# Kernel tuning notes

Measured on AMD Instinct MI355X. Metric: run time of the kernel, lower is better.

The kernel has to match this reference:

```python
import jax, jax.numpy as jnp
import numpy as np

DIVERSITY_RATE = 0.5


def setup_inputs() -> dict:
    key = jax.random.key(0)
    k1, k2 = jax.random.split(key)
    # model log-probabilities at current step: (bsz, beam, vocab)
    lprobs = jax.nn.log_softmax(
        jax.random.normal(k1, (128, 5, 50257), dtype=jnp.float32), axis=-1
    )
    # historical hypothesis scores: (bsz, beam, step)
    scores = jax.random.normal(k2, (128, 5, 10), dtype=jnp.float32)
    return {"lprobs": lprobs, "scores": scores, "step": 10}


def reference(lprobs, scores, step):
    bsz, beam_size, vocab_size = lprobs.shape
    k = min(beam_size * 2, beam_size * vocab_size - 1)  # = 10 here

    # step > 0 path: accumulate running score of each hypothesis
    lp = lprobs + scores[:, :, step - 1][:, :, None]  # (bsz, beam, vocab)

    # 1/ per-beam top-k over vocab (vectorized over all beams at once)
    s, idx = jax.lax.top_k(lp, k)  # (bsz, beam, k); idx already < vocab (fmod no-op)

    # 2/,3/ intra-sibling ordering -> rank penalty (rank r gets r*rate)
    sibling_score = jnp.arange(1, k + 1, dtype=lp.dtype) * DIVERSITY_RATE  # (k,)
    s = s - sibling_score  # broadcast over (bsz, beam, k)

    # 4/ final top-k over all beam*k candidates
    indices = idx.reshape(bsz, beam_size * k)
    final_scores, flat_pos = jax.lax.top_k(s.reshape(bsz, beam_size * k), k)
    final_beams = flat_pos // k  # which input beam each winner came from
    final_indices = jnp.take_along_axis(indices, flat_pos, axis=1)  # vocab ids

    return final_scores, final_indices, final_beams
```

## Files before the change

kernel.cpp:

```cpp
#include <hip/hip_runtime.h>
#include <hip/hip_bf16.h>
#include <math.h>
#include <stdint.h>


#define BS    256
#define KK    10
#define BEAM  5
#define CS    7168
#define NSLOT 7
#define CAP   2048
#define FCAP  2048

typedef unsigned long long u64;

__device__ __forceinline__ uint32_t ford(float x) {
    uint32_t u = __float_as_uint(x);
    return (u & 0x80000000u) ? ~u : (u | 0x80000000u);
}
__device__ __forceinline__ float funord(uint32_t u) {
    return __uint_as_float((u & 0x80000000u) ? (u & 0x7fffffffu) : ~u);
}

__device__ __forceinline__ void insert10(u64 (&key)[KK], u64 k) {
    if (k > key[KK - 1]) {
#pragma unroll
        for (int j = KK - 1; j >= 1; --j)
            key[j] = (k > key[j - 1]) ? key[j - 1] : ((k > key[j]) ? k : key[j]);
        if (k > key[0]) key[0] = k;
    }
}

__global__ __launch_bounds__(BS) void dss_chunk_topk(
    const float* __restrict__ lprobs,
    const float* __restrict__ scores,
    const int*   __restrict__ step_ptr,
    int vocab, int sdim, int nc,
    u64* __restrict__ ws_keys)
{
    const int chunk = blockIdx.x;
    const int row   = blockIdx.y;
    const int tid   = threadIdx.x;
    const int lane  = tid & 63;
    const int step  = step_ptr[0];
    const float bias = scores[(size_t)row * sdim + (step - 1)];

    const int c0 = chunk * CS;
    int len = vocab - c0; if (len > CS) len = CS;
    const float* cp = lprobs + (size_t)row * vocab + c0;

    __shared__ u64  cand[CAP];
    __shared__ int  s_cnt;
    __shared__ float s_tau;

    int pre = (4 - (int)(((uintptr_t)cp >> 2) & 3)) & 3;
    if (pre > len) pre = len;
    const float4* g4 = (const float4*)(cp + pre);
    const int nvec = (len - pre) >> 2;
    const int done = pre + 4 * nvec;
    const int rem  = len - done;

    float4 v[NSLOT];
    float m = -INFINITY;
#pragma unroll
    for (int i = 0; i < NSLOT; ++i) {
        int idx = tid + (i << 8);
        if (idx < nvec) {
            float4 x = g4[idx];
            x.x += bias; x.y += bias; x.z += bias; x.w += bias;
            v[i] = x;
            m = fmaxf(m, fmaxf(fmaxf(x.x, x.y), fmaxf(x.z, x.w)));
        } else {
            v[i].x = -INFINITY; v[i].y = -INFINITY; v[i].z = -INFINITY; v[i].w = -INFINITY;
        }
    }
    float xv = -INFINITY; int xi = -1;
    if (tid < pre)                        { xi = tid;            xv = cp[xi] + bias; }
    else if (tid >= 4 && tid < 4 + rem)   { xi = done + tid - 4; xv = cp[xi] + bias; }
    m = fmaxf(m, xv);

    if (tid == 0) s_cnt = 0;

    if (tid < 64) {
        float s = m;
#pragma unroll
        for (int k2 = 2; k2 <= 64; k2 <<= 1) {
#pragma unroll
            for (int j = k2 >> 1; j >= 1; j >>= 1) {
                float p = __shfl_xor(s, j);
                bool lower   = (lane & j) == 0;
                bool dirDesc = (lane & k2) == 0;
                s = (dirDesc == lower) ? fmaxf(s, p) : fminf(s, p);
            }
        }
        if (lane == 9) s_tau = s;
    }
    __syncthreads();
    const float tau = s_tau;

    auto app = [&](float x, int j) {
        if (j < len) {
            int p = atomicAdd(&s_cnt, 1);
            if (p < CAP) cand[p] = ((u64)ford(x) << 32) | (uint32_t)~(c0 + j);
        }
    };
#pragma unroll
    for (int i = 0; i < NSLOT; ++i) {
        int base = pre + ((tid + (i << 8)) << 2);
        if (v[i].x >= tau) app(v[i].x, base + 0);
        if (v[i].y >= tau) app(v[i].y, base + 1);
        if (v[i].z >= tau) app(v[i].z, base + 2);
        if (v[i].w >= tau) app(v[i].w, base + 3);
    }
    if (xi >= 0 && xv >= tau) app(xv, xi);
    __syncthreads();

    if (tid < 64) {
        int n = s_cnt; if (n > CAP) n = CAP;
        u64* outp = ws_keys + ((size_t)row * nc + chunk) * KK;
        if (n <= 64) {
            u64 k = (lane < n) ? cand[lane] : 0;
#pragma unroll
            for (int k2 = 2; k2 <= 64; k2 <<= 1) {
#pragma unroll
                for (int j = k2 >> 1; j >= 1; j >>= 1) {
                    u64 p = __shfl_xor(k, j);
                    bool lower   = (lane & j) == 0;
                    bool dirDesc = (lane & k2) == 0;
                    bool wantMax = (dirDesc == lower);
                    k = wantMax ? (k > p ? k : p) : (k < p ? k : p);
                }
            }
            if (lane < KK) outp[lane] = k;
        } else {
            u64 key[KK];
#pragma unroll
            for (int j = 0; j < KK; ++j) key[j] = 0;
            for (int i = lane; i < n; i += 64) insert10(key, cand[i]);
#pragma unroll
            for (int r = 0; r < KK; ++r) {
                u64 rv = key[0]; int rl = lane;
#pragma unroll
                for (int o = 32; o >= 1; o >>= 1) {
                    u64 ov = __shfl_xor(rv, o);
                    int ol = __shfl_xor(rl, o);
                    if (ov > rv || (ov == rv && ol < rl)) { rv = ov; rl = ol; }
                }
                if (lane == rl) {
#pragma unroll
                    for (int j = 0; j < KK - 1; ++j) key[j] = key[j + 1];
                    key[KK - 1] = 0;
                }
                if (lane == 0) outp[r] = rv;
            }
        }
    }
}

__global__ __launch_bounds__(BS) void dss_row_topk(
    const float* __restrict__ lprobs,
    const float* __restrict__ scores,
    const int*   __restrict__ step_ptr,
    int vocab, int sdim,
    u64* __restrict__ ws_keys)
{
    const int row = blockIdx.x;
    const int tid = threadIdx.x;
    const int step = step_ptr[0];
    const float bias = scores[(size_t)row * sdim + (step - 1)];
    const float* rp = lprobs + (size_t)row * vocab;

    __shared__ u64  cand[FCAP];
    __shared__ u64  skey[BS * KK];
    __shared__ int  cnt;
    __shared__ float sh_tau;

    int pre = (4 - (int)(((uintptr_t)rp >> 2) & 3)) & 3;
    if (pre > vocab) pre = vocab;
    const float4* p4 = (const float4*)(rp + pre);
    const int nvec = (vocab - pre) >> 2;
    const int done = pre + 4 * nvec;
    const int rem  = vocab - done;

    float m = -INFINITY;
    if (tid < pre) m = rp[tid] + bias;
    for (int t = tid; t < nvec; t += BS) {
        float4 x = p4[t];
        m = fmaxf(m, fmaxf(fmaxf(x.x + bias, x.y + bias), fmaxf(x.z + bias, x.w + bias)));
    }
    if (tid < rem) m = fmaxf(m, rp[done + tid] + bias);

    skey[tid * KK] = ((u64)ford(m) << 32) | (uint32_t)~tid;
#pragma unroll
    for (int j = 1; j < KK; ++j) skey[tid * KK + j] = 0;
    if (tid == 0) cnt = 0;
    __syncthreads();
    for (int off = BS / 2; off >= 1; off >>= 1) {
        if (tid < off) {
            const int pa = tid * KK, pb = (tid + off) * KK;
            u64 mk[KK]; int ia = 0, ib = 0;
#pragma unroll
            for (int j = 0; j < KK; ++j) {
                u64 ka = skey[pa + ia], kb = skey[pb + ib];
                bool tA = (ka >= kb); mk[j] = tA ? ka : kb;
                if (tA) ++ia; else ++ib;
            }
#pragma unroll
            for (int j = 0; j < KK; ++j) skey[pa + j] = mk[j];
        }
        __syncthreads();
    }
    if (tid == 0) sh_tau = funord((uint32_t)(skey[9] >> 32));
    __syncthreads();
    const float tau = sh_tau;

    auto app = [&](float x, int i) {
        if (x >= tau) {
            int p = atomicAdd(&cnt, 1);
            if (p < FCAP) cand[p] = ((u64)ford(x) << 32) | (uint32_t)~i;
        }
    };
    if (tid < pre) app(rp[tid] + bias, tid);
    for (int t = tid; t < nvec; t += BS) {
        float4 x = p4[t];
        int base = pre + 4 * t;
        app(x.x + bias, base + 0); app(x.y + bias, base + 1);
        app(x.z + bias, base + 2); app(x.w + bias, base + 3);
    }
    if (tid < rem) app(rp[done + tid] + bias, done + tid);
    __syncthreads();

    const int n = (cnt < FCAP) ? cnt : FCAP;
    {
        u64 key[KK];
#pragma unroll
        for (int j = 0; j < KK; ++j) key[j] = 0;
        for (int i = tid; i < n; i += BS) insert10(key, cand[i]);
#pragma unroll
        for (int j = 0; j < KK; ++j) skey[tid * KK + j] = key[j];
    }
    __syncthreads();
    for (int off = BS / 2; off >= 1; off >>= 1) {
        if (tid < off) {
            const int pa = tid * KK, pb = (tid + off) * KK;
            u64 mk[KK]; int ia = 0, ib = 0;
#pragma unroll
            for (int j = 0; j < KK; ++j) {
                u64 ka = skey[pa + ia], kb = skey[pb + ib];
                bool tA = (ka >= kb); mk[j] = tA ? ka : kb;
                if (tA) ++ia; else ++ib;
            }
#pragma unroll
            for (int j = 0; j < KK; ++j) skey[pa + j] = mk[j];
        }
        __syncthreads();
    }
    if (tid < KK) ws_keys[(size_t)row * KK + tid] = skey[tid];
}

__global__ __launch_bounds__(BEAM * 64) void dss_final(
    const u64* __restrict__ ws_keys,
    float* __restrict__ out, int bsz, int nc)
{
    const int b    = blockIdx.x;
    const int beam = threadIdx.x >> 6;
    const int lane = threadIdx.x & 63;

    __shared__ float s_pen[BEAM * KK];
    __shared__ int   s_idx[BEAM * KK];

    const int ncand = nc * KK;
    const u64* kp = ws_keys + (size_t)(b * BEAM + beam) * ncand;
    u64 c0 = (lane < ncand) ? kp[lane] : 0;
    u64 c1 = (lane + 64 < ncand) ? kp[lane + 64] : 0;

#pragma unroll
    for (int r = 0; r < KK; ++r) {
        u64 my = (c0 > c1) ? c0 : c1;
        u64 rv = my; int rl = lane;
#pragma unroll
        for (int o = 32; o >= 1; o >>= 1) {
            u64 ov = __shfl_xor(rv, o);
            int ol = __shfl_xor(rl, o);
            if (ov > rv || (ov == rv && ol < rl)) { rv = ov; rl = ol; }
        }
        if (lane == rl) { if (c0 == rv) c0 = 0; else c1 = 0; }
        if (lane == 0) {
            s_pen[beam * KK + r] = funord((uint32_t)(rv >> 32)) - 0.5f * (float)(r + 1);
            s_idx[beam * KK + r] = (int)~(uint32_t)rv;
        }
    }
    __syncthreads();

    if (threadIdx.x < 64) {
        float v = -INFINITY; int vidx = 0;
        if (lane < BEAM * KK) { v = s_pen[lane]; vidx = s_idx[lane]; }
        float* out_scores  = out;
        float* out_indices = out + (size_t)bsz * KK;
        float* out_beams   = out + 2 * (size_t)bsz * KK;
        for (int o = 0; o < KK; ++o) {
            float rv = v; int rp = lane;
#pragma unroll
            for (int off = 32; off >= 1; off >>= 1) {
                float ov = __shfl_xor(rv, off);
                int   op = __shfl_xor(rp, off);
                if (ov > rv || (ov == rv && op < rp)) { rv = ov; rp = op; }
            }
            int widx = __shfl(vidx, rp);
            if (lane == 0) {
                out_scores [b * KK + o] = rv;
                out_indices[b * KK + o] = (float)widx;
                out_beams  [b * KK + o] = (float)(rp / KK);
            }
            if (lane == rp) v = -INFINITY;
        }
    }
}

extern "C" void kernel_launch(void* const* d_in, const int* in_sizes, int n_in,
                              void* d_out, int out_size, void* d_ws, size_t ws_size,
                              hipStream_t stream)
{
    const float* lprobs = (const float*)d_in[0];
    const float* scores = (const float*)d_in[1];
    const int*   step   = (const int*)d_in[2];

    const int bsz   = 128;
    const int rows  = bsz * BEAM;
    const int vocab = in_sizes[0] / rows;
    const int sdim  = in_sizes[1] / rows;

    u64* ws_keys = (u64*)d_ws;

    int nc = (vocab + CS - 1) / CS;
    if (ws_size < (size_t)rows * nc * KK * sizeof(u64)) nc = 1;

    if (nc > 1) {
        dss_chunk_topk<<<dim3(nc, rows), BS, 0, stream>>>(
            lprobs, scores, step, vocab, sdim, nc, ws_keys);
    } else {
        dss_row_topk<<<rows, BS, 0, stream>>>(lprobs, scores, step, vocab, sdim, ws_keys);
    }
    dss_final<<<bsz, BEAM * 64, 0, stream>>>(ws_keys, (float*)d_out, bsz, nc);
}
```

Measured before the change: 211.9 us.

## Replace bitonic sorts and shuffle argmax loops with rank-counting selection

```diff
diff --git a/kernel.cpp b/kernel.cpp
--- a/kernel.cpp
+++ b/kernel.cpp
@@ -9,7 +9,7 @@
 #define BEAM  5
 #define CS    7168
 #define NSLOT 7
-#define CAP   2048
+#define CAP   1024
 #define FCAP  2048
 
 typedef unsigned long long u64;
@@ -51,7 +51,6 @@
 
     __shared__ u64  cand[CAP];
     __shared__ int  s_cnt;
-    __shared__ float s_tau;
 
     int pre = (4 - (int)(((uintptr_t)cp >> 2) & 3)) & 3;
     if (pre > len) pre = len;
@@ -81,22 +80,17 @@
 
     if (tid == 0) s_cnt = 0;
 
-    if (tid < 64) {
-        float s = m;
-#pragma unroll
-        for (int k2 = 2; k2 <= 64; k2 <<= 1) {
-#pragma unroll
-            for (int j = k2 >> 1; j >= 1; j >>= 1) {
-                float p = __shfl_xor(s, j);
-                bool lower   = (lane & j) == 0;
-                bool dirDesc = (lane & k2) == 0;
-                s = (dirDesc == lower) ? fmaxf(s, p) : fminf(s, p);
-            }
-        }
-        if (lane == 9) s_tau = s;
-    }
-    __syncthreads();
-    const float tau = s_tau;
+    int r = 0;
+    const int mb = __float_as_int(m);
+    for (int j = 0; j < 64; ++j) {
+        float vj = __int_as_float(__builtin_amdgcn_readlane(mb, j));
+        r += (vj > m || (vj == m && j < lane)) ? 1 : 0;
+    }
+    u64 msk = __ballot(r == 9);
+    int src = __ffsll((long long)msk) - 1;
+    const float tau = __int_as_float(__builtin_amdgcn_readlane(mb, src));
+
+    __syncthreads();
 
     auto app = [&](float x, int j) {
         if (j < len) {
@@ -115,45 +109,13 @@
     if (xi >= 0 && xv >= tau) app(xv, xi);
     __syncthreads();
 
-    if (tid < 64) {
-        int n = s_cnt; if (n > CAP) n = CAP;
-        u64* outp = ws_keys + ((size_t)row * nc + chunk) * KK;
-        if (n <= 64) {
-            u64 k = (lane < n) ? cand[lane] : 0;
-#pragma unroll
-            for (int k2 = 2; k2 <= 64; k2 <<= 1) {
-#pragma unroll
-                for (int j = k2 >> 1; j >= 1; j >>= 1) {
-                    u64 p = __shfl_xor(k, j);
-                    bool lower   = (lane & j) == 0;
-                    bool dirDesc = (lane & k2) == 0;
-                    bool wantMax = (dirDesc == lower);
-                    k = wantMax ? (k > p ? k : p) : (k < p ? k : p);
-                }
-            }
-            if (lane < KK) outp[lane] = k;
-        } else {
-            u64 key[KK];
-#pragma unroll
-            for (int j = 0; j < KK; ++j) key[j] = 0;
-            for (int i = lane; i < n; i += 64) insert10(key, cand[i]);
-#pragma unroll
-            for (int r = 0; r < KK; ++r) {
-                u64 rv = key[0]; int rl = lane;
-#pragma unroll
-                for (int o = 32; o >= 1; o >>= 1) {
-                    u64 ov = __shfl_xor(rv, o);
-                    int ol = __shfl_xor(rl, o);
-                    if (ov > rv || (ov == rv && ol < rl)) { rv = ov; rl = ol; }
-                }
-                if (lane == rl) {
-#pragma unroll
-                    for (int j = 0; j < KK - 1; ++j) key[j] = key[j + 1];
-                    key[KK - 1] = 0;
-                }
-                if (lane == 0) outp[r] = rv;
-            }
-        }
+    int n = s_cnt; if (n > CAP) n = CAP;
+    u64* outp = ws_keys + ((size_t)row * nc + chunk) * KK;
+    for (int t = tid; t < n; t += BS) {
+        u64 k = cand[t];
+        int rk = 0;
+        for (int j = 0; j < n; ++j) rk += (cand[j] > k) ? 1 : 0;
+        if (rk < KK) outp[rk] = k;
     }
 }
 
@@ -258,61 +220,46 @@
     if (tid < KK) ws_keys[(size_t)row * KK + tid] = skey[tid];
 }
 
-__global__ __launch_bounds__(BEAM * 64) void dss_final(
+__global__ __launch_bounds__(512) void dss_final(
     const u64* __restrict__ ws_keys,
     float* __restrict__ out, int bsz, int nc)
 {
-    const int b    = blockIdx.x;
-    const int beam = threadIdx.x >> 6;
-    const int lane = threadIdx.x & 63;
-
-    __shared__ float s_pen[BEAM * KK];
-    __shared__ int   s_idx[BEAM * KK];
-
-    const int ncand = nc * KK;
-    const u64* kp = ws_keys + (size_t)(b * BEAM + beam) * ncand;
-    u64 c0 = (lane < ncand) ? kp[lane] : 0;
-    u64 c1 = (lane + 64 < ncand) ? kp[lane + 64] : 0;
-
-#pragma unroll
-    for (int r = 0; r < KK; ++r) {
-        u64 my = (c0 > c1) ? c0 : c1;
-        u64 rv = my; int rl = lane;
-#pragma unroll
-        for (int o = 32; o >= 1; o >>= 1) {
-            u64 ov = __shfl_xor(rv, o);
-            int ol = __shfl_xor(rl, o);
-            if (ov > rv || (ov == rv && ol < rl)) { rv = ov; rl = ol; }
-        }
-        if (lane == rl) { if (c0 == rv) c0 = 0; else c1 = 0; }
-        if (lane == 0) {
-            s_pen[beam * KK + r] = funord((uint32_t)(rv >> 32)) - 0.5f * (float)(r + 1);
-            s_idx[beam * KK + r] = (int)~(uint32_t)rv;
-        }
-    }
-    __syncthreads();
-
-    if (threadIdx.x < 64) {
-        float v = -INFINITY; int vidx = 0;
-        if (lane < BEAM * KK) { v = s_pen[lane]; vidx = s_idx[lane]; }
-        float* out_scores  = out;
-        float* out_indices = out + (size_t)bsz * KK;
-        float* out_beams   = out + 2 * (size_t)bsz * KK;
-        for (int o = 0; o < KK; ++o) {
-            float rv = v; int rp = lane;
-#pragma unroll
-            for (int off = 32; off >= 1; off >>= 1) {
-                float ov = __shfl_xor(rv, off);
-                int   op = __shfl_xor(rp, off);
-                if (ov > rv || (ov == rv && op < rp)) { rv = ov; rp = op; }
-            }
-            int widx = __shfl(vidx, rp);
-            if (lane == 0) {
-                out_scores [b * KK + o] = rv;
-                out_indices[b * KK + o] = (float)widx;
-                out_beams  [b * KK + o] = (float)(rp / KK);
-            }
-            if (lane == rp) v = -INFINITY;
+    const int b = blockIdx.x;
+    const int t = threadIdx.x;
+    const int NC  = nc * KK;
+    const int tot = BEAM * NC;
+
+    __shared__ u64  kbuf[BEAM * KK * 8];
+    __shared__ float pen[BEAM * KK];
+    __shared__ int   pidx[BEAM * KK];
+
+    for (int i = t; i < tot; i += 512) kbuf[i] = ws_keys[(size_t)b * tot + i];
+    __syncthreads();
+
+    if (t < tot) {
+        int beam = t / NC;
+        u64 k = kbuf[t];
+        const u64* kb = kbuf + beam * NC;
+        int r = 0;
+        for (int j = 0; j < NC; ++j) r += (kb[j] > k) ? 1 : 0;
+        if (r < KK) {
+            pen [beam * KK + r] = funord((uint32_t)(k >> 32)) - 0.5f * (float)(r + 1);
+            pidx[beam * KK + r] = (int)~(uint32_t)k;
+        }
+    }
+    __syncthreads();
+
+    if (t < BEAM * KK) {
+        float p = pen[t];
+        int r = 0;
+        for (int j = 0; j < BEAM * KK; ++j) {
+            float q = pen[j];
+            r += (q > p || (q == p && j < t)) ? 1 : 0;
+        }
+        if (r < KK) {
+            out[              b * KK + r] = p;
+            out[(size_t)bsz * KK     + b * KK + r] = (float)pidx[t];
+            out[(size_t)2 * bsz * KK + b * KK + r] = (float)(t / KK);
         }
     }
 }
@@ -333,6 +280,7 @@
     u64* ws_keys = (u64*)d_ws;
 
     int nc = (vocab + CS - 1) / CS;
+    if (nc > 8) nc = 8;
     if (ws_size < (size_t)rows * nc * KK * sizeof(u64)) nc = 1;
 
     if (nc > 1) {
@@ -341,5 +289,5 @@
     } else {
         dss_row_topk<<<rows, BS, 0, stream>>>(lprobs, scores, step, vocab, sdim, ws_keys);
     }
-    dss_final<<<bsz, BEAM * 64, 0, stream>>>(ws_keys, (float*)d_out, bsz, nc);
-}
+    dss_final<<<bsz, 512, 0, stream>>>(ws_keys, (float*)d_out, bsz, nc);
+}
```

New measurement: 200.2 us. -5.5%, faster.
